# Kernel tuning notes

Measured on AMD Instinct MI355X. Metric: run time of the kernel, lower is better.

The kernel has to match this reference:

```python
import jax, jax.numpy as jnp
import numpy as np

TEMPERATURE = 0.07
NORM_EPS = 1e-12   # F.normalize eps
LOG_EPS = 1e-08


def setup_inputs() -> dict:
    key = jax.random.key(0)
    k1, k2 = jax.random.split(key)
    N, D, C = 8192, 512, 64
    projections = jax.random.normal(k1, (N, D), dtype=jnp.float32)
    targets = jax.random.randint(k2, (N,), 0, C, dtype=jnp.int64)
    return {"projections": projections, "targets": targets}


def reference(projections, targets):
    # L2-normalize rows (matches F.normalize: x / max(||x||, eps))
    norm = jnp.linalg.norm(projections, axis=1, keepdims=True)
    p = projections / jnp.maximum(norm, NORM_EPS)

    # [N, N] cosine similarity / temperature
    sim = jnp.matmul(p, p.T) / TEMPERATURE
    # row-max subtraction for numerical stability (gradient flows through max,
    # as in the torch original)
    sim = sim - jnp.max(sim, axis=1, keepdims=True)
    exp_sim = jnp.exp(sim)

    n = projections.shape[0]
    eye = jnp.eye(n, dtype=bool)
    mask_self = ~eye                                   # exclude self-pairs
    mask_pos = (targets[:, None] == targets[None, :]) & mask_self

    denom = jnp.sum(jnp.where(mask_self, exp_sim, 0.0), axis=1, keepdims=True)
    log_prob = sim - jnp.log(denom + LOG_EPS)

    num = jnp.sum(jnp.where(mask_pos, log_prob, 0.0), axis=1)
    cnt = jnp.sum(mask_pos, axis=1).astype(log_prob.dtype)
    # divide_no_nan: 0 where cnt == 0
    loss_per_sample = jnp.where(cnt == 0, 0.0, num / jnp.where(cnt == 0, 1.0, cnt))
    return loss_per_sample
```

## Files before the change

### kernel.cpp

```cpp
#include <hip/hip_runtime.h>
#include <hip/hip_bf16.h>
#include <math.h>

#define N_ROWS 8192
#define DIM    512
#define NCLS   64
#define BM     256
#define BK     64
#define NKT    (DIM / BK)
#define NTILE  (N_ROWS / BM)
#define NTRI   (NTILE * (NTILE + 1) / 2)
#define NSLOT  NTILE
#define M_CONST 14.285714285714286f
#define SCALE_SQRT 3.7796447300922722f

using bf16x8 = __attribute__((ext_vector_type(8))) short;
using f32x4  = __attribute__((ext_vector_type(4))) float;

static __device__ inline unsigned short f2bf(float x) {
  unsigned u = __float_as_uint(x);
  unsigned r = u + 0x7FFFu + ((u >> 16) & 1u);
  return (unsigned short)(r >> 16);
}

__global__ __launch_bounds__(256) void normalize_rows(const float* __restrict__ proj,
                                                      unsigned short* __restrict__ outb) {
  const int row  = blockIdx.x * 4 + (threadIdx.x >> 6);
  const int lane = threadIdx.x & 63;
  const float4* src = (const float4*)(proj + (size_t)row * DIM);
  float4 a = src[lane * 2];
  float4 b = src[lane * 2 + 1];
  float ss = a.x*a.x + a.y*a.y + a.z*a.z + a.w*a.w
           + b.x*b.x + b.y*b.y + b.z*b.z + b.w*b.w;
#pragma unroll
  for (int off = 1; off < 64; off <<= 1) ss += __shfl_xor(ss, off);
  const float scale = SCALE_SQRT / fmaxf(sqrtf(ss), 1e-12f);
  float v[8] = {a.x, a.y, a.z, a.w, b.x, b.y, b.z, b.w};
  unsigned short h[8];
#pragma unroll
  for (int i = 0; i < 8; ++i) h[i] = f2bf(v[i] * scale);
  uint4 packed;
  packed.x = (unsigned)h[0] | ((unsigned)h[1] << 16);
  packed.y = (unsigned)h[2] | ((unsigned)h[3] << 16);
  packed.z = (unsigned)h[4] | ((unsigned)h[5] << 16);
  packed.w = (unsigned)h[6] | ((unsigned)h[7] << 16);
  *(uint4*)(outb + (size_t)row * DIM + lane * 8) = packed;
}

__global__ __launch_bounds__(1024) void class_hist(const int* __restrict__ tgt,
                                                   int* __restrict__ hist) {
  __shared__ int h[16][NCLS];
  const int wid = threadIdx.x >> 6;
  const int lane = threadIdx.x & 63;
  if (lane < NCLS) h[wid][lane] = 0;
  __syncthreads();
  for (int i = threadIdx.x; i < N_ROWS; i += 1024) atomicAdd(&h[wid][tgt[i]], 1);
  __syncthreads();
  if (threadIdx.x < NCLS) {
    int s = 0;
#pragma unroll
    for (int w = 0; w < 16; ++w) s += h[w][threadIdx.x];
    hist[threadIdx.x] = s;
  }
}

__global__ __launch_bounds__(512, 2) void supcon_tile(const unsigned short* __restrict__ p16,
                                                      const int* __restrict__ tgt,
                                                      float* __restrict__ dpart,
                                                      float* __restrict__ spart) {
  const int logical = ((int)blockIdx.x & 7) * (NTRI / 8) + ((int)blockIdx.x >> 3);
  int rem = logical, br = 0;
  while (rem >= NTILE - br) { rem -= NTILE - br; ++br; }
  const int bc = br + rem;

  __shared__ short As[2][BM * BK];
  __shared__ short Bs[2][BM * BK];
  __shared__ int   tgr[BM], tgc[BM];
  __shared__ float redE[4][BM], redS[4][BM];
  __shared__ float redEc[2][BM], redSc[2][BM];

  const int tid  = threadIdx.x;
  const int lane = tid & 63;
  const int wid  = tid >> 6;
  const int wm = wid >> 2, wn = wid & 3;
  const int lhi = lane >> 4, llo = lane & 15;

  const size_t rowA0 = (size_t)br * BM;
  const size_t rowB0 = (size_t)bc * BM;

#define STAGE_HALF(XS, BUF, ROW0, H, KT) do {                                   \
  _Pragma("unroll")                                                             \
  for (int j = 0; j < 2; ++j) {                                                 \
    const int g  = wid * 64 + lane + j * 512;                                   \
    const int r  = (H) * 128 + (g >> 3);                                        \
    const int gl = (g & 7) ^ (r & 7);                                           \
    const unsigned short* src = p16 + ((ROW0) + r) * DIM + (KT) * BK + gl * 8;  \
    __builtin_amdgcn_global_load_lds(                                           \
        (const __attribute__((address_space(1))) void*)src,                     \
        (__attribute__((address_space(3))) void*)&XS[BUF][(H) * 8192 + g * 8],  \
        16, 0, 0);                                                              \
  }                                                                             \
} while (0)

#define STAGE_TILE(BUF, KT) do {          \
  STAGE_HALF(As, BUF, rowA0, 0, KT);      \
  STAGE_HALF(As, BUF, rowA0, 1, KT);      \
  STAGE_HALF(Bs, BUF, rowB0, 0, KT);      \
  STAGE_HALF(Bs, BUF, rowB0, 1, KT);      \
} while (0)

  const int tg0 = (tid < BM) ? tgt[br * BM + tid] : tgt[bc * BM + (tid - BM)];
  STAGE_TILE(0, 0);
  if (tid < BM) tgr[tid] = tg0;
  else          tgc[tid - BM] = tg0;

  f32x4 zero = {0.f, 0.f, 0.f, 0.f};
  f32x4 acc[8][4];
#pragma unroll
  for (int i = 0; i < 8; ++i)
#pragma unroll
    for (int j = 0; j < 4; ++j) acc[i][j] = zero;

#pragma unroll
  for (int kt = 0; kt < NKT; ++kt) {
    const int cur = kt & 1, nxt = cur ^ 1;

    if (kt + 1 < NKT) {
      STAGE_TILE(nxt, kt + 1);
      asm volatile("s_waitcnt vmcnt(8)");
    } else {
      asm volatile("s_waitcnt vmcnt(0)");
    }
    __builtin_amdgcn_sched_barrier(0);
    __builtin_amdgcn_s_barrier();
    __builtin_amdgcn_sched_barrier(0);

    bf16x8 bfr[4][2];
#pragma unroll
    for (int ni = 0; ni < 4; ++ni)
#pragma unroll
      for (int ks = 0; ks < 2; ++ks) {
        const int Rb = wn * 64 + ni * 16 + llo;
        bfr[ni][ks] = *(const bf16x8*)&Bs[cur][Rb * BK + (((ks * 4 + lhi) ^ (Rb & 7)) * 8)];
      }

#pragma unroll
    for (int ph = 0; ph < 4; ++ph) {
      const int h = ph >> 1, ks = ph & 1;
      bf16x8 af[4];
#pragma unroll
      for (int mi = 0; mi < 4; ++mi) {
        const int Ra = wm * 128 + h * 64 + mi * 16 + llo;
        af[mi] = *(const bf16x8*)&As[cur][Ra * BK + (((ks * 4 + lhi) ^ (Ra & 7)) * 8)];
      }
      asm volatile("s_waitcnt lgkmcnt(0)");
      __builtin_amdgcn_sched_barrier(0);
      __builtin_amdgcn_s_setprio(1);
#pragma unroll
      for (int mi = 0; mi < 4; ++mi)
#pragma unroll
        for (int ni = 0; ni < 4; ++ni)
          acc[h * 4 + mi][ni] =
              __builtin_amdgcn_mfma_f32_16x16x32_bf16(af[mi], bfr[ni][ks], acc[h * 4 + mi][ni], 0, 0, 0);
      __builtin_amdgcn_s_setprio(0);
      __builtin_amdgcn_s_barrier();
    }
  }
#undef STAGE_TILE
#undef STAGE_HALF

  const bool diag = (br == bc);
  float ecol[4] = {0.f, 0.f, 0.f, 0.f};
  float scol[4] = {0.f, 0.f, 0.f, 0.f};

#pragma unroll
  for (int mi = 0; mi < 8; ++mi) {
#pragma unroll
    for (int rg = 0; rg < 4; ++rg) {
      const int rin  = wm * 128 + mi * 16 + lhi * 4 + rg;
      const int trow = tgr[rin];
      float esum = 0.f, ssum = 0.f;
#pragma unroll
      for (int ni = 0; ni < 4; ++ni) {
        const int cin = wn * 64 + ni * 16 + llo;
        const float sim = acc[mi][ni][rg];
        const bool self = diag && (rin == cin);
        const float e = self ? 0.f : __expf(sim - M_CONST);
        const bool pos = (!self) && (trow == tgc[cin]);
        const float sv = pos ? sim : 0.f;
        esum += e;  ssum += sv;
        ecol[ni] += e;  scol[ni] += sv;
      }
#pragma unroll
      for (int off = 1; off < 16; off <<= 1) {
        esum += __shfl_xor(esum, off);
        ssum += __shfl_xor(ssum, off);
      }
      if (llo == 0) { redE[wn][rin] = esum; redS[wn][rin] = ssum; }
    }
  }
  if (!diag) {
#pragma unroll
    for (int ni = 0; ni < 4; ++ni) {
      float ec = ecol[ni], sc = scol[ni];
      ec += __shfl_xor(ec, 16); ec += __shfl_xor(ec, 32);
      sc += __shfl_xor(sc, 16); sc += __shfl_xor(sc, 32);
      if (lhi == 0) {
        redEc[wm][wn * 64 + ni * 16 + llo] = ec;
        redSc[wm][wn * 64 + ni * 16 + llo] = sc;
      }
    }
  }
  __syncthreads();

  if (tid < BM) {
    const float e = redE[0][tid] + redE[1][tid] + redE[2][tid] + redE[3][tid];
    const float s = redS[0][tid] + redS[1][tid] + redS[2][tid] + redS[3][tid];
    dpart[(size_t)bc * N_ROWS + rowA0 + tid] = e;
    spart[(size_t)bc * N_ROWS + rowA0 + tid] = s;
  } else if (!diag) {
    const int c = tid - BM;
    dpart[(size_t)br * N_ROWS + rowB0 + c] = redEc[0][c] + redEc[1][c];
    spart[(size_t)br * N_ROWS + rowB0 + c] = redSc[0][c] + redSc[1][c];
  }
}

__global__ __launch_bounds__(256) void combine_loss(const float* __restrict__ dpart,
                                                    const float* __restrict__ spart,
                                                    const int* __restrict__ tgt,
                                                    const int* __restrict__ hist,
                                                    float* __restrict__ out) {
  __shared__ float dsh[4][64], ssh[4][64];
  const int lane = threadIdx.x & 63;
  const int g    = threadIdx.x >> 6;
  const int r    = blockIdx.x * 64 + lane;
  float d = 0.f, s = 0.f;
  for (int k = g * (NSLOT / 4); k < (g + 1) * (NSLOT / 4); ++k) {
    d += dpart[(size_t)k * N_ROWS + r];
    s += spart[(size_t)k * N_ROWS + r];
  }
  dsh[g][lane] = d; ssh[g][lane] = s;
  __syncthreads();
  if (g == 0) {
    d = dsh[0][lane] + dsh[1][lane] + dsh[2][lane] + dsh[3][lane];
    s = ssh[0][lane] + ssh[1][lane] + ssh[2][lane] + ssh[3][lane];
    const int cnt = hist[tgt[r]] - 1;
    out[r] = (cnt > 0) ? (s / (float)cnt - M_CONST - logf(d + 1e-8f)) : 0.f;
  }
}

extern "C" void kernel_launch(void* const* d_in, const int* in_sizes, int n_in,
                              void* d_out, int out_size, void* d_ws, size_t ws_size,
                              hipStream_t stream) {
  const float* proj = (const float*)d_in[0];
  const int*   tgt  = (const int*)d_in[1];
  float* out = (float*)d_out;

  char* ws = (char*)d_ws;
  unsigned short* p16  = (unsigned short*)ws;
  float* dpart = (float*)(ws + (size_t)8 * 1024 * 1024);
  float* spart = (float*)(ws + (size_t)9 * 1024 * 1024);
  int*   hist  = (int*)(ws + (size_t)10 * 1024 * 1024);

  normalize_rows<<<N_ROWS / 4, 256, 0, stream>>>(proj, p16);
  class_hist<<<1, 1024, 0, stream>>>(tgt, hist);
  supcon_tile<<<NTRI, 512, 0, stream>>>(p16, tgt, dpart, spart);
  combine_loss<<<N_ROWS / 64, 256, 0, stream>>>(dpart, spart, tgt, hist, out);
}
```

Baseline: 105.1 us.

## Restructure tile pipeline with phase-interleaved staging and exp2-scaled similarities

Reworks the MFMA main loop so each phase loads its own A and B fragments, and spreads the next k-tile's global-to-LDS staging across phases 0 and 1. The wait on global loads moves to the end of the last phase. Folding log2(e) into the normalization scale lets the epilogue use a raw exp2 instead of expf, and the final kernel divides it back out. It also drops the occupancy hint from launch bounds and caches the column targets in registers. This aims to overlap loads with compute and cut epilogue ALU work, at the cost of a different register and occupancy profile plus a more fragile ordering of barriers and waits.

```diff
diff --git a/kernel.cpp b/kernel.cpp
--- a/kernel.cpp
+++ b/kernel.cpp
@@ -12,7 +12,9 @@
 #define NTRI   (NTILE * (NTILE + 1) / 2)
 #define NSLOT  NTILE
 #define M_CONST 14.285714285714286f
-#define SCALE_SQRT 3.7796447300922722f
+#define L2E     1.4426950408889634f
+#define M2_CONST 20.60992915555662f
+#define SCALE2  4.539815541256959f
 
 using bf16x8 = __attribute__((ext_vector_type(8))) short;
 using f32x4  = __attribute__((ext_vector_type(4))) float;
@@ -34,7 +36,7 @@
            + b.x*b.x + b.y*b.y + b.z*b.z + b.w*b.w;
 #pragma unroll
   for (int off = 1; off < 64; off <<= 1) ss += __shfl_xor(ss, off);
-  const float scale = SCALE_SQRT / fmaxf(sqrtf(ss), 1e-12f);
+  const float scale = SCALE2 / fmaxf(sqrtf(ss), 1e-12f);
   float v[8] = {a.x, a.y, a.z, a.w, b.x, b.y, b.z, b.w};
   unsigned short h[8];
 #pragma unroll
@@ -64,10 +66,10 @@
   }
 }
 
-__global__ __launch_bounds__(512, 2) void supcon_tile(const unsigned short* __restrict__ p16,
-                                                      const int* __restrict__ tgt,
-                                                      float* __restrict__ dpart,
-                                                      float* __restrict__ spart) {
+__global__ __launch_bounds__(512) void supcon_tile(const unsigned short* __restrict__ p16,
+                                                   const int* __restrict__ tgt,
+                                                   float* __restrict__ dpart,
+                                                   float* __restrict__ spart) {
   const int logical = ((int)blockIdx.x & 7) * (NTRI / 8) + ((int)blockIdx.x >> 3);
   int rem = logical, br = 0;
   while (rem >= NTILE - br) { rem -= NTILE - br; ++br; }
@@ -88,31 +90,22 @@
   const size_t rowA0 = (size_t)br * BM;
   const size_t rowB0 = (size_t)bc * BM;
 
-#define STAGE_HALF(XS, BUF, ROW0, H, KT) do {                                   \
+#define STAGE_ARR(XS, BUF, ROW0, KT) do {                                       \
   _Pragma("unroll")                                                             \
-  for (int j = 0; j < 2; ++j) {                                                 \
-    const int g  = wid * 64 + lane + j * 512;                                   \
-    const int r  = (H) * 128 + (g >> 3);                                        \
-    const int gl = (g & 7) ^ (r & 7);                                           \
+  for (int j = 0; j < 4; ++j) {                                                 \
+    const int g  = tid + j * 512;                                               \
+    const int r  = g >> 3, gp = g & 7;                                          \
+    const int gl = gp ^ (r & 7);                                                \
     const unsigned short* src = p16 + ((ROW0) + r) * DIM + (KT) * BK + gl * 8;  \
-    __builtin_amdgcn_global_load_lds(                                           \
-        (const __attribute__((address_space(1))) void*)src,                     \
-        (__attribute__((address_space(3))) void*)&XS[BUF][(H) * 8192 + g * 8],  \
-        16, 0, 0);                                                              \
+    __builtin_amdgcn_global_load_lds((const __attribute__((address_space(1))) void*)src, \
+        (__attribute__((address_space(3))) void*)&XS[BUF][g * 8], 16, 0, 0);    \
   }                                                                             \
 } while (0)
 
-#define STAGE_TILE(BUF, KT) do {          \
-  STAGE_HALF(As, BUF, rowA0, 0, KT);      \
-  STAGE_HALF(As, BUF, rowA0, 1, KT);      \
-  STAGE_HALF(Bs, BUF, rowB0, 0, KT);      \
-  STAGE_HALF(Bs, BUF, rowB0, 1, KT);      \
-} while (0)
-
-  const int tg0 = (tid < BM) ? tgt[br * BM + tid] : tgt[bc * BM + (tid - BM)];
-  STAGE_TILE(0, 0);
-  if (tid < BM) tgr[tid] = tg0;
-  else          tgc[tid - BM] = tg0;
+  STAGE_ARR(As, 0, rowA0, 0);
+  STAGE_ARR(Bs, 0, rowB0, 0);
+  if (tid < BM) tgr[tid] = tgt[br * BM + tid];
+  else          tgc[tid - BM] = tgt[bc * BM + (tid - BM)];
 
   f32x4 zero = {0.f, 0.f, 0.f, 0.f};
   f32x4 acc[8][4];
@@ -121,55 +114,63 @@
 #pragma unroll
     for (int j = 0; j < 4; ++j) acc[i][j] = zero;
 
+  __syncthreads();
+
 #pragma unroll
   for (int kt = 0; kt < NKT; ++kt) {
     const int cur = kt & 1, nxt = cur ^ 1;
-
-    if (kt + 1 < NKT) {
-      STAGE_TILE(nxt, kt + 1);
-      asm volatile("s_waitcnt vmcnt(8)");
-    } else {
-      asm volatile("s_waitcnt vmcnt(0)");
-    }
-    __builtin_amdgcn_sched_barrier(0);
-    __builtin_amdgcn_s_barrier();
-    __builtin_amdgcn_sched_barrier(0);
-
-    bf16x8 bfr[4][2];
-#pragma unroll
-    for (int ni = 0; ni < 4; ++ni)
-#pragma unroll
-      for (int ks = 0; ks < 2; ++ks) {
-        const int Rb = wn * 64 + ni * 16 + llo;
-        bfr[ni][ks] = *(const bf16x8*)&Bs[cur][Rb * BK + (((ks * 4 + lhi) ^ (Rb & 7)) * 8)];
-      }
-
 #pragma unroll
     for (int ph = 0; ph < 4; ++ph) {
-      const int h = ph >> 1, ks = ph & 1;
-      bf16x8 af[4];
+      const int mh = ph >> 1, nh = ph & 1;
+
+      bf16x8 af[4][2], bf[2][2];
 #pragma unroll
       for (int mi = 0; mi < 4; ++mi) {
-        const int Ra = wm * 128 + h * 64 + mi * 16 + llo;
-        af[mi] = *(const bf16x8*)&As[cur][Ra * BK + (((ks * 4 + lhi) ^ (Ra & 7)) * 8)];
-      }
-      asm volatile("s_waitcnt lgkmcnt(0)");
+        const int Ra = wm * 128 + mh * 64 + mi * 16 + llo;
+#pragma unroll
+        for (int ks = 0; ks < 2; ++ks)
+          af[mi][ks] = *(const bf16x8*)&As[cur][Ra * BK + (((ks * 4 + lhi) ^ (Ra & 7)) * 8)];
+      }
+#pragma unroll
+      for (int ni = 0; ni < 2; ++ni) {
+        const int Rb = wn * 64 + nh * 32 + ni * 16 + llo;
+#pragma unroll
+        for (int ks = 0; ks < 2; ++ks)
+          bf[ni][ks] = *(const bf16x8*)&Bs[cur][Rb * BK + (((ks * 4 + lhi) ^ (Rb & 7)) * 8)];
+      }
+
+      if (kt + 1 < NKT) {
+        if (ph == 0)      STAGE_ARR(As, nxt, rowA0, kt + 1);
+        else if (ph == 1) STAGE_ARR(Bs, nxt, rowB0, kt + 1);
+      }
+
+      __builtin_amdgcn_s_barrier();
+      asm volatile("s_waitcnt lgkmcnt(0)" ::: "memory");
       __builtin_amdgcn_sched_barrier(0);
       __builtin_amdgcn_s_setprio(1);
 #pragma unroll
-      for (int mi = 0; mi < 4; ++mi)
-#pragma unroll
-        for (int ni = 0; ni < 4; ++ni)
-          acc[h * 4 + mi][ni] =
-              __builtin_amdgcn_mfma_f32_16x16x32_bf16(af[mi], bfr[ni][ks], acc[h * 4 + mi][ni], 0, 0, 0);
+      for (int ks = 0; ks < 2; ++ks)
+#pragma unroll
+        for (int mi = 0; mi < 4; ++mi)
+#pragma unroll
+          for (int ni = 0; ni < 2; ++ni)
+            acc[mh * 4 + mi][nh * 2 + ni] =
+                __builtin_amdgcn_mfma_f32_16x16x32_bf16(af[mi][ks], bf[ni][ks],
+                                                        acc[mh * 4 + mi][nh * 2 + ni], 0, 0, 0);
       __builtin_amdgcn_s_setprio(0);
+      if (ph == 3) {
+        asm volatile("s_waitcnt vmcnt(0)" ::: "memory");
+        __builtin_amdgcn_sched_barrier(0);
+      }
       __builtin_amdgcn_s_barrier();
     }
   }
-#undef STAGE_TILE
-#undef STAGE_HALF
+#undef STAGE_ARR
 
   const bool diag = (br == bc);
+  int tc[4];
+#pragma unroll
+  for (int ni = 0; ni < 4; ++ni) tc[ni] = tgc[wn * 64 + ni * 16 + llo];
   float ecol[4] = {0.f, 0.f, 0.f, 0.f};
   float scol[4] = {0.f, 0.f, 0.f, 0.f};
 
@@ -183,11 +184,11 @@
 #pragma unroll
       for (int ni = 0; ni < 4; ++ni) {
         const int cin = wn * 64 + ni * 16 + llo;
-        const float sim = acc[mi][ni][rg];
+        const float x = acc[mi][ni][rg];
         const bool self = diag && (rin == cin);
-        const float e = self ? 0.f : __expf(sim - M_CONST);
-        const bool pos = (!self) && (trow == tgc[cin]);
-        const float sv = pos ? sim : 0.f;
+        const float e = self ? 0.f : __builtin_amdgcn_exp2f(x - M2_CONST);
+        const bool pos = (!self) && (trow == tc[ni]);
+        const float sv = pos ? x : 0.f;
         esum += e;  ssum += sv;
         ecol[ni] += e;  scol[ni] += sv;
       }
@@ -245,7 +246,7 @@
     d = dsh[0][lane] + dsh[1][lane] + dsh[2][lane] + dsh[3][lane];
     s = ssh[0][lane] + ssh[1][lane] + ssh[2][lane] + ssh[3][lane];
     const int cnt = hist[tgt[r]] - 1;
-    out[r] = (cnt > 0) ? (s / (float)cnt - M_CONST - logf(d + 1e-8f)) : 0.f;
+    out[r] = (cnt > 0) ? (s / (L2E * (float)cnt) - M_CONST - logf(d + 1e-8f)) : 0.f;
   }
 }
 
```

New measurement: 107.0 us. About the same (+1.8%).
